# Kernel optimization log

Measured on AMD Instinct MI355X. Metric: run time of the kernel, lower is better.

## Reference

```python
import jax, jax.numpy as jnp
import numpy as np

EMB, HID, SEQ, BATCH, VOCAB, NLAYERS = 512, 512, 64, 64, 10000, 2


def setup_inputs() -> dict:
    key = jax.random.key(0)
    ks = jax.random.split(key, 8)
    u = lambda k, s: jax.random.uniform(k, s, jnp.float32, -0.1, 0.1)
    return {
        "inputs": jax.random.randint(ks[0], (SEQ, BATCH), 0, VOCAB),  # (S,B) token ids
        "hidden": jnp.zeros((NLAYERS, BATCH, HID), jnp.float32),      # init_hidden()
        "emb": u(ks[1], (VOCAB, EMB)),                                # embedding table
        "W0": u(ks[2], (HID, EMB)),  "bW0": jnp.zeros((HID,), jnp.float32),
        "W1": u(ks[3], (HID, HID)), "bW1": jnp.zeros((HID,), jnp.float32),
        "U0": u(ks[4], (HID, HID)), "bU0": jnp.zeros((HID,), jnp.float32),
        "U1": u(ks[5], (HID, HID)), "bU1": jnp.zeros((HID,), jnp.float32),
        "Wd": u(ks[6], (VOCAB, HID)), "bd": jnp.zeros((VOCAB,), jnp.float32),
    }


def reference(inputs, hidden, emb, W0, bW0, W1, bW1, U0, bU0, U1, bU1, Wd, bd):
    # Stacked 2-layer Elman RNN; dp_keep_prob=1.0 -> dropout is identity.
    x = emb[inputs]  # (S,B,E) embedding lookup for all timesteps at once

    def step(h, x_t):
        # h: (2,B,H); x_t: (B,E)
        h0 = jnp.tanh(x_t @ W0.T + bW0 + h[0] @ U0.T + bU0)   # layer 0
        h1 = jnp.tanh(h0 @ W1.T + bW1 + h[1] @ U1.T + bU1)    # layer 1
        logits = h1 @ Wd.T + bd                                # (B,V)
        return jnp.stack([h0, h1]), logits

    h_final, logits = jax.lax.scan(step, hidden, x)
    return logits, h_final  # (S,B,V), (2,B,H)
```

## Files before the change

### kernel.cpp

```cpp
#include <hip/hip_runtime.h>
#include <hip/hip_bf16.h>
#include <hip/hip_fp16.h>


typedef _Float16 f16;
typedef _Float16 f16x8 __attribute__((ext_vector_type(8)));
typedef float fvec4 __attribute__((ext_vector_type(4)));
typedef float f32x4 __attribute__((ext_vector_type(4)));

__device__ __forceinline__ f32x4 mfma16(f16x8 a, f16x8 b, f32x4 c) {
    return __builtin_amdgcn_mfma_f32_16x16x32_f16(a, b, c, 0, 0, 0);
}

__device__ __forceinline__ f16x8 cvt_f16x8(fvec4 a, fvec4 b) {
    f16x8 r;
    r[0] = (f16)a[0]; r[1] = (f16)a[1]; r[2] = (f16)a[2]; r[3] = (f16)a[3];
    r[4] = (f16)b[0]; r[5] = (f16)b[1]; r[6] = (f16)b[2]; r[7] = (f16)b[3];
    return r;
}

__global__ void cvt_f32_f16(const float* __restrict__ src, f16* __restrict__ dst, int n8) {
    int i = blockIdx.x * 256 + threadIdx.x;
    if (i >= n8) return;
    const fvec4* p = (const fvec4*)(src + (size_t)i * 8);
    *(f16x8*)(dst + (size_t)i * 8) = cvt_f16x8(p[0], p[1]);
}

__global__ void cvt_wd(const float* __restrict__ src, f16* __restrict__ dst) {
    int i = blockIdx.x * 256 + threadIdx.x;
    if (i >= 647168) return;
    if (i < 640000) {
        const fvec4* p = (const fvec4*)(src + (size_t)i * 8);
        *(f16x8*)(dst + (size_t)i * 8) = cvt_f16x8(p[0], p[1]);
    } else {
        f16x8 z = {};
        *(f16x8*)(dst + (size_t)i * 8) = z;
    }
}

__global__ void gather_x(const int* __restrict__ toks, const float* __restrict__ emb,
                         f16* __restrict__ xb) {
    int i = blockIdx.x * 256 + threadIdx.x;
    if (i >= 262144) return;
    int row = i >> 6, seg = i & 63;
    int tok = toks[row];
    const fvec4* p = (const fvec4*)(emb + (size_t)tok * 512 + seg * 8);
    *(f16x8*)(xb + (size_t)row * 512 + seg * 8) = cvt_f16x8(p[0], p[1]);
}

__global__ __launch_bounds__(256) void gemm_bt(
    const f16* __restrict__ A, const f16* __restrict__ Bm,
    const float* __restrict__ bias1, const float* __restrict__ bias2,
    float* __restrict__ C, int N)
{
    const int tM = blockIdx.x * 128;
    const int tN = blockIdx.y * 128;
    const int tid = threadIdx.x;
    const int l = tid & 63, w = tid >> 6;
    const int wr = w >> 1, wc = w & 1;
    const int l15 = l & 15, l4 = l >> 4;

    __shared__ f16 As[128 * 40];
    __shared__ f16 Bs[128 * 40];

    f32x4 acc[4][4] = {};

    for (int ks = 0; ks < 16; ++ks) {
        const int k0 = ks * 32;
        __syncthreads();
#pragma unroll
        for (int it = 0; it < 2; ++it) {
            int c = tid + it * 256;
            int row = c >> 2, seg = c & 3;
            *(f16x8*)(&As[row * 40 + seg * 8]) =
                *(const f16x8*)(A + (size_t)(tM + row) * 512 + k0 + seg * 8);
            *(f16x8*)(&Bs[row * 40 + seg * 8]) =
                *(const f16x8*)(Bm + (size_t)(tN + row) * 512 + k0 + seg * 8);
        }
        __syncthreads();
        f16x8 af[4], bf[4];
#pragma unroll
        for (int m = 0; m < 4; ++m)
            af[m] = *(const f16x8*)(&As[(wr * 64 + m * 16 + l15) * 40 + 8 * l4]);
#pragma unroll
        for (int n = 0; n < 4; ++n)
            bf[n] = *(const f16x8*)(&Bs[(wc * 64 + n * 16 + l15) * 40 + 8 * l4]);
#pragma unroll
        for (int m = 0; m < 4; ++m)
#pragma unroll
            for (int n = 0; n < 4; ++n)
                acc[m][n] = mfma16(af[m], bf[n], acc[m][n]);
    }

#pragma unroll
    for (int n = 0; n < 4; ++n) {
        int col = tN + wc * 64 + n * 16 + l15;
        if (col >= N) continue;
        float bsum = (bias1 ? bias1[col] : 0.f) + (bias2 ? bias2[col] : 0.f);
#pragma unroll
        for (int m = 0; m < 4; ++m) {
#pragma unroll
            for (int r = 0; r < 4; ++r) {
                int row = tM + wr * 64 + m * 16 + l4 * 4 + r;
                C[(size_t)row * N + col] = acc[m][n][r] + bsum;
            }
        }
    }
}

__global__ __launch_bounds__(512, 2) void recur_kernel(
    const float* __restrict__ Ain,
    const float* __restrict__ U,
    const float* __restrict__ h0,
    f16* __restrict__ Hh,
    float* __restrict__ outTail)
{
    const int g = blockIdx.x;
    const int tid = threadIdx.x;
    const int l = tid & 63, w = tid >> 6;
    const int l15 = l & 15, l4 = l >> 4;
    const int colbase = w * 64;

    __shared__ __align__(16) char smem[17408 + 131072];
    f16*  hs   = (f16*)smem;
    char* ldsB = smem + 17408;

    f16x8 bf[4][12];
#pragma unroll
    for (int nt = 0; nt < 4; ++nt) {
        const float* urow = U + (size_t)(colbase + nt * 16 + l15) * 512 + 8 * l4;
#pragma unroll
        for (int kk = 0; kk < 12; ++kk) {
            const fvec4* p = (const fvec4*)(urow + kk * 32);
            bf[nt][kk] = cvt_f16x8(p[0], p[1]);
        }
#pragma unroll
        for (int kk = 12; kk < 16; ++kk) {
            const fvec4* p = (const fvec4*)(urow + kk * 32);
            *(f16x8*)(ldsB + ((w * 4 + nt) * 4 + (kk - 12)) * 1024 + l * 16) =
                cvt_f16x8(p[0], p[1]);
        }
    }
    for (int c = tid; c < 1024; c += 512) {
        int row = c >> 6, seg = c & 63;
        const fvec4* p = (const fvec4*)(h0 + (size_t)(g * 16 + row) * 512 + seg * 8);
        *(f16x8*)((char*)hs + row * 1088 + seg * 16) = cvt_f16x8(p[0], p[1]);
    }
    __syncthreads();

    for (int t = 0; t < 64; ++t) {
        float ain[16];
        const float* abase = Ain + ((size_t)t * 64 + g * 16) * 512;
#pragma unroll
        for (int nt = 0; nt < 4; ++nt)
#pragma unroll
            for (int r = 0; r < 4; ++r)
                ain[nt * 4 + r] = abase[(l4 * 4 + r) * 512 + colbase + nt * 16 + l15];

        f32x4 acc[4] = {};
        const char* arow = (const char*)hs + l15 * 1088 + l4 * 16;
#pragma unroll
        for (int kk = 0; kk < 12; ++kk) {
            f16x8 a = *(const f16x8*)(arow + kk * 64);
            acc[0] = mfma16(a, bf[0][kk], acc[0]);
            acc[1] = mfma16(a, bf[1][kk], acc[1]);
            acc[2] = mfma16(a, bf[2][kk], acc[2]);
            acc[3] = mfma16(a, bf[3][kk], acc[3]);
        }
#pragma unroll
        for (int kk = 12; kk < 16; ++kk) {
            f16x8 a = *(const f16x8*)(arow + kk * 64);
#pragma unroll
            for (int nt = 0; nt < 4; ++nt) {
                f16x8 b = *(const f16x8*)(ldsB + ((w * 4 + nt) * 4 + (kk - 12)) * 1024 + l * 16);
                acc[nt] = mfma16(a, b, acc[nt]);
            }
        }

#pragma unroll
        for (int nt = 0; nt < 4; ++nt)
#pragma unroll
            for (int r = 0; r < 4; ++r) {
                float x = acc[nt][r] + ain[nt * 4 + r];
                float e = __expf(2.0f * x);
                ain[nt * 4 + r] = 1.0f - 2.0f * __builtin_amdgcn_rcpf(e + 1.0f);
            }

        __syncthreads();
#pragma unroll
        for (int nt = 0; nt < 4; ++nt)
#pragma unroll
            for (int r = 0; r < 4; ++r)
                hs[(l4 * 4 + r) * 544 + colbase + nt * 16 + l15] = (f16)ain[nt * 4 + r];
        __syncthreads();

        f16* hrow = Hh + ((size_t)t * 64 + g * 16) * 512;
        for (int c = tid; c < 1024; c += 512) {
            int row = c >> 6, seg = c & 63;
            *(f16x8*)(hrow + (size_t)row * 512 + seg * 8) =
                *(const f16x8*)((const char*)hs + row * 1088 + seg * 16);
        }
        if (t == 63) {
#pragma unroll
            for (int nt = 0; nt < 4; ++nt)
#pragma unroll
                for (int r = 0; r < 4; ++r)
                    outTail[(size_t)(g * 16 + l4 * 4 + r) * 512 + colbase + nt * 16 + l15] =
                        ain[nt * 4 + r];
        }
    }
}

extern "C" void kernel_launch(void* const* d_in, const int* in_sizes, int n_in,
                              void* d_out, int out_size, void* d_ws, size_t ws_size,
                              hipStream_t stream) {
    const int*   toks   = (const int*)d_in[0];
    const float* hidden = (const float*)d_in[1];
    const float* emb    = (const float*)d_in[2];
    const float* W0  = (const float*)d_in[3];
    const float* bW0 = (const float*)d_in[4];
    const float* W1  = (const float*)d_in[5];
    const float* bW1 = (const float*)d_in[6];
    const float* U0  = (const float*)d_in[7];
    const float* bU0 = (const float*)d_in[8];
    const float* U1  = (const float*)d_in[9];
    const float* bU1 = (const float*)d_in[10];
    const float* Wd  = (const float*)d_in[11];
    const float* bd  = (const float*)d_in[12];
    float* out = (float*)d_out;

    char* ws = (char*)d_ws;
    f16*   W0h  = (f16*)(ws + 0);
    f16*   W1h  = (f16*)(ws + 524288);
    f16*   Wdh  = (f16*)(ws + 1048576);
    f16*   Xb   = (f16*)(ws + 11403264);
    f16*   H0h  = (f16*)(ws + 15597568);
    f16*   H1h  = (f16*)(ws + 19791872);
    float* A0   = (float*)(ws + 23986176);
    float* B1   = (float*)(ws + 32374784);

    cvt_f32_f16<<<128, 256, 0, stream>>>(W0, W0h, 32768);
    cvt_f32_f16<<<128, 256, 0, stream>>>(W1, W1h, 32768);
    cvt_wd<<<2528, 256, 0, stream>>>(Wd, Wdh);
    gather_x<<<1024, 256, 0, stream>>>(toks, emb, Xb);

    gemm_bt<<<dim3(32, 4), 256, 0, stream>>>(Xb, W0h, bW0, bU0, A0, 512);
    recur_kernel<<<4, 512, 0, stream>>>(A0, U0, hidden, H0h, out + 40960000);
    gemm_bt<<<dim3(32, 4), 256, 0, stream>>>(H0h, W1h, bW1, bU1, B1, 512);
    recur_kernel<<<4, 512, 0, stream>>>(B1, U1, hidden + 32768, H1h,
                                        out + 40960000 + 32768);
    gemm_bt<<<dim3(32, 79), 256, 0, stream>>>(H1h, Wdh, bd, nullptr, out, 10000);
}
```

Before: 484.9 us.

## Transpose recurrence MFMA, double-buffer swizzled hidden state, prepack input projection layout

The recurrent kernel now computes U·h instead of h·U, so each lane holds four consecutive output columns of one row. That lets it write packed f16 results straight to a double-buffered, XOR-swizzled LDS hidden state and to global memory, which removes one of the two barriers per step and the separate copy-out pass. The input-projection GEMM gains a mode that writes its output in a per-lane packed layout, so each step loads the precomputed activations as contiguous vector loads instead of strided scalars. This adds layout coupling between the GEMM and the recurrence, and the f16 conversion now uses round-toward-zero packing.

Result: slower. 497.9 us (+2.7%).

```diff
diff --git a/kernel.cpp b/kernel.cpp
--- a/kernel.cpp
+++ b/kernel.cpp
@@ -4,9 +4,12 @@
 
 
 typedef _Float16 f16;
+typedef _Float16 f16x2 __attribute__((ext_vector_type(2)));
 typedef _Float16 f16x8 __attribute__((ext_vector_type(8)));
 typedef float fvec4 __attribute__((ext_vector_type(4)));
 typedef float f32x4 __attribute__((ext_vector_type(4)));
+typedef unsigned int u32;
+typedef u32 u32x2 __attribute__((ext_vector_type(2)));
 
 __device__ __forceinline__ f32x4 mfma16(f16x8 a, f16x8 b, f32x4 c) {
     return __builtin_amdgcn_mfma_f32_16x16x32_f16(a, b, c, 0, 0, 0);
@@ -48,6 +51,7 @@
     *(f16x8*)(xb + (size_t)row * 512 + seg * 8) = cvt_f16x8(p[0], p[1]);
 }
 
+template <int MODE>
 __global__ __launch_bounds__(256) void gemm_bt(
     const f16* __restrict__ A, const f16* __restrict__ Bm,
     const float* __restrict__ bias1, const float* __restrict__ bias2,
@@ -92,24 +96,45 @@
                 acc[m][n] = mfma16(af[m], bf[n], acc[m][n]);
     }
 
-#pragma unroll
-    for (int n = 0; n < 4; ++n) {
-        int col = tN + wc * 64 + n * 16 + l15;
-        if (col >= N) continue;
-        float bsum = (bias1 ? bias1[col] : 0.f) + (bias2 ? bias2[col] : 0.f);
-#pragma unroll
-        for (int m = 0; m < 4; ++m) {
-#pragma unroll
-            for (int r = 0; r < 4; ++r) {
-                int row = tM + wr * 64 + m * 16 + l4 * 4 + r;
-                C[(size_t)row * N + col] = acc[m][n][r] + bsum;
+    if (MODE == 0) {
+#pragma unroll
+        for (int n = 0; n < 4; ++n) {
+            int col = tN + wc * 64 + n * 16 + l15;
+            if (col >= N) continue;
+            float bsum = (bias1 ? bias1[col] : 0.f) + (bias2 ? bias2[col] : 0.f);
+#pragma unroll
+            for (int m = 0; m < 4; ++m)
+#pragma unroll
+                for (int r = 0; r < 4; ++r) {
+                    int row = tM + wr * 64 + m * 16 + l4 * 4 + r;
+                    C[(size_t)row * N + col] = acc[m][n][r] + bsum;
+                }
+        }
+    } else {
+        const int t  = blockIdx.x * 2 + wr;
+        const int wp = blockIdx.y * 2 + wc;
+        const int lp_hi = (l15 >> 2) * 16;
+        const int rp = l15 & 3;
+#pragma unroll
+        for (int n = 0; n < 4; ++n) {
+            int col = tN + wc * 64 + n * 16 + l15;
+            float bsum = bias1[col] + bias2[col];
+#pragma unroll
+            for (int m = 0; m < 4; ++m) {
+#pragma unroll
+                for (int r = 0; r < 4; ++r) {
+                    int lanep = lp_hi + l4 * 4 + r;
+                    size_t idx = ((((size_t)t * 4 + m) * 8 + wp) * 64 + lanep) * 16
+                                 + n * 4 + rp;
+                    C[idx] = acc[m][n][r] + bsum;
+                }
             }
         }
     }
 }
 
 __global__ __launch_bounds__(512, 2) void recur_kernel(
-    const float* __restrict__ Ain,
+    const float* __restrict__ A0p,
     const float* __restrict__ U,
     const float* __restrict__ h0,
     f16* __restrict__ Hh,
@@ -121,9 +146,9 @@
     const int l15 = l & 15, l4 = l >> 4;
     const int colbase = w * 64;
 
-    __shared__ __align__(16) char smem[17408 + 131072];
-    f16*  hs   = (f16*)smem;
-    char* ldsB = smem + 17408;
+    __shared__ __align__(16) char smem[163840];
+    char* hsb  = smem;
+    char* ldsB = smem + 32768;
 
     f16x8 bf[4][12];
 #pragma unroll
@@ -133,6 +158,7 @@
         for (int kk = 0; kk < 12; ++kk) {
             const fvec4* p = (const fvec4*)(urow + kk * 32);
             bf[nt][kk] = cvt_f16x8(p[0], p[1]);
+            asm volatile("" : "+v"(bf[nt][kk]));
         }
 #pragma unroll
         for (int kk = 12; kk < 16; ++kk) {
@@ -144,70 +170,61 @@
     for (int c = tid; c < 1024; c += 512) {
         int row = c >> 6, seg = c & 63;
         const fvec4* p = (const fvec4*)(h0 + (size_t)(g * 16 + row) * 512 + seg * 8);
-        *(f16x8*)((char*)hs + row * 1088 + seg * 16) = cvt_f16x8(p[0], p[1]);
+        *(f16x8*)(hsb + row * 1024 + ((seg * 16) ^ ((row & 7) << 4))) =
+            cvt_f16x8(p[0], p[1]);
     }
     __syncthreads();
 
+    const int sw = (l15 & 7) << 4;
+    const int rowbase = l15 * 1024;
+
     for (int t = 0; t < 64; ++t) {
-        float ain[16];
-        const float* abase = Ain + ((size_t)t * 64 + g * 16) * 512;
-#pragma unroll
-        for (int nt = 0; nt < 4; ++nt)
-#pragma unroll
-            for (int r = 0; r < 4; ++r)
-                ain[nt * 4 + r] = abase[(l4 * 4 + r) * 512 + colbase + nt * 16 + l15];
-
+        const float* ab = A0p + (((size_t)t * 4 + g) * 8 + w) * 1024 + l * 16;
+        f32x4 ain[4];
+#pragma unroll
+        for (int nt = 0; nt < 4; ++nt) ain[nt] = *(const fvec4*)(ab + nt * 4);
+
+        const char* hrd = hsb + (t & 1) * 16384 + rowbase;
         f32x4 acc[4] = {};
-        const char* arow = (const char*)hs + l15 * 1088 + l4 * 16;
 #pragma unroll
         for (int kk = 0; kk < 12; ++kk) {
-            f16x8 a = *(const f16x8*)(arow + kk * 64);
-            acc[0] = mfma16(a, bf[0][kk], acc[0]);
-            acc[1] = mfma16(a, bf[1][kk], acc[1]);
-            acc[2] = mfma16(a, bf[2][kk], acc[2]);
-            acc[3] = mfma16(a, bf[3][kk], acc[3]);
+            f16x8 h = *(const f16x8*)(hrd + ((kk * 64 + l4 * 16) ^ sw));
+            acc[0] = mfma16(bf[0][kk], h, acc[0]);
+            acc[1] = mfma16(bf[1][kk], h, acc[1]);
+            acc[2] = mfma16(bf[2][kk], h, acc[2]);
+            acc[3] = mfma16(bf[3][kk], h, acc[3]);
         }
 #pragma unroll
         for (int kk = 12; kk < 16; ++kk) {
-            f16x8 a = *(const f16x8*)(arow + kk * 64);
+            f16x8 h = *(const f16x8*)(hrd + ((kk * 64 + l4 * 16) ^ sw));
 #pragma unroll
             for (int nt = 0; nt < 4; ++nt) {
-                f16x8 b = *(const f16x8*)(ldsB + ((w * 4 + nt) * 4 + (kk - 12)) * 1024 + l * 16);
-                acc[nt] = mfma16(a, b, acc[nt]);
+                f16x8 u = *(const f16x8*)(ldsB + ((w * 4 + nt) * 4 + (kk - 12)) * 1024 + l * 16);
+                acc[nt] = mfma16(u, h, acc[nt]);
             }
         }
 
-#pragma unroll
-        for (int nt = 0; nt < 4; ++nt)
+        char* hwr = hsb + (((t & 1) ^ 1) * 16384) + rowbase;
+        f16* hrow = Hh + ((size_t)t * 64 + g * 16 + l15) * 512;
+#pragma unroll
+        for (int nt = 0; nt < 4; ++nt) {
+            f32x4 v;
 #pragma unroll
             for (int r = 0; r < 4; ++r) {
-                float x = acc[nt][r] + ain[nt * 4 + r];
+                float x = acc[nt][r] + ain[nt][r];
                 float e = __expf(2.0f * x);
-                ain[nt * 4 + r] = 1.0f - 2.0f * __builtin_amdgcn_rcpf(e + 1.0f);
+                v[r] = 1.0f - 2.0f * __builtin_amdgcn_rcpf(e + 1.0f);
             }
-
+            u32 p0 = __builtin_bit_cast(u32, __builtin_amdgcn_cvt_pkrtz(v[0], v[1]));
+            u32 p1 = __builtin_bit_cast(u32, __builtin_amdgcn_cvt_pkrtz(v[2], v[3]));
+            u32x2 pk; pk[0] = p0; pk[1] = p1;
+            int c0 = colbase + nt * 16 + l4 * 4;
+            *(u32x2*)(hwr + ((c0 * 2) ^ sw)) = pk;
+            *(u32x2*)(hrow + c0) = pk;
+            if (t == 63)
+                *(f32x4*)(outTail + (size_t)(g * 16 + l15) * 512 + c0) = v;
+        }
         __syncthreads();
-#pragma unroll
-        for (int nt = 0; nt < 4; ++nt)
-#pragma unroll
-            for (int r = 0; r < 4; ++r)
-                hs[(l4 * 4 + r) * 544 + colbase + nt * 16 + l15] = (f16)ain[nt * 4 + r];
-        __syncthreads();
-
-        f16* hrow = Hh + ((size_t)t * 64 + g * 16) * 512;
-        for (int c = tid; c < 1024; c += 512) {
-            int row = c >> 6, seg = c & 63;
-            *(f16x8*)(hrow + (size_t)row * 512 + seg * 8) =
-                *(const f16x8*)((const char*)hs + row * 1088 + seg * 16);
-        }
-        if (t == 63) {
-#pragma unroll
-            for (int nt = 0; nt < 4; ++nt)
-#pragma unroll
-                for (int r = 0; r < 4; ++r)
-                    outTail[(size_t)(g * 16 + l4 * 4 + r) * 512 + colbase + nt * 16 + l15] =
-                        ain[nt * 4 + r];
-        }
     }
 }
 
@@ -244,10 +261,10 @@
     cvt_wd<<<2528, 256, 0, stream>>>(Wd, Wdh);
     gather_x<<<1024, 256, 0, stream>>>(toks, emb, Xb);
 
-    gemm_bt<<<dim3(32, 4), 256, 0, stream>>>(Xb, W0h, bW0, bU0, A0, 512);
+    gemm_bt<1><<<dim3(32, 4), 256, 0, stream>>>(Xb, W0h, bW0, bU0, A0, 512);
     recur_kernel<<<4, 512, 0, stream>>>(A0, U0, hidden, H0h, out + 40960000);
-    gemm_bt<<<dim3(32, 4), 256, 0, stream>>>(H0h, W1h, bW1, bU1, B1, 512);
+    gemm_bt<1><<<dim3(32, 4), 256, 0, stream>>>(H0h, W1h, bW1, bU1, B1, 512);
     recur_kernel<<<4, 512, 0, stream>>>(B1, U1, hidden + 32768, H1h,
                                         out + 40960000 + 32768);
-    gemm_bt<<<dim3(32, 79), 256, 0, stream>>>(H1h, Wdh, bd, nullptr, out, 10000);
-}
+    gemm_bt<0><<<dim3(32, 79), 256, 0, stream>>>(H1h, Wdh, bd, nullptr, out, 10000);
+}
```
